# Performance work log

Hardware: AMD Instinct MI355X
Metric: run time of the kernel (lower is better)

The kernel has to match this reference:

```python
import jax, jax.numpy as jnp
import numpy as np

NUM_CLASSES = 101
BATCH = 262144
LAMBDA = 1000.0


def setup_inputs() -> dict:
    key = jax.random.key(0)
    k1, k2 = jax.random.split(key)
    outputs = jax.random.normal(k1, (BATCH, NUM_CLASSES), dtype=jnp.float32)
    targets = jax.random.randint(k2, (BATCH,), 0, NUM_CLASSES, dtype=jnp.int64)
    return {"outputs": outputs, "targets": targets}


def reference(outputs, targets):
    B, C = outputs.shape
    targets = targets.reshape(-1)
    tf = targets.astype(outputs.dtype)

    probs = jax.nn.softmax(outputs, axis=1)                      # [B, C]
    labels = jnp.arange(C, dtype=outputs.dtype)                  # [C]
    pred_values = jnp.sum(probs * labels[None, :], axis=1)       # [B]
    centered = labels[None, :] - pred_values[:, None]            # [B, C]
    variance = jnp.sum(probs * centered * centered, axis=1)      # [B]
    variance = jnp.clip(variance, 1e-6, None)
    est_err = (pred_values - tf) ** 2
    concentrated_loss = jnp.mean(0.5 * jnp.log(variance) + est_err / (2.0 * variance))

    # Unimodal ordinal penalty, vectorized over the original double loop:
    # sign_j = -1 if j < target else +1; penalty = relu(-(p_j - p_{j+1}) * sign_j)
    j = jnp.arange(C - 1)                                        # [C-1]
    sign = jnp.where(j[None, :] < targets[:, None], -1.0, 1.0).astype(outputs.dtype)
    prob_diff = probs[:, :-1] - probs[:, 1:]                     # [B, C-1]
    penalty = jax.nn.relu(-prob_diff * sign)
    unimodal_loss = jnp.sum(penalty) / B
    weighted_unimodal_loss = LAMBDA * unimodal_loss

    total_loss = concentrated_loss + weighted_unimodal_loss
    return (total_loss, concentrated_loss, weighted_unimodal_loss)
```

## Files before the change

### kernel.cpp

```cpp
#include <hip/hip_runtime.h>


#define NC 101
#define LAMBDA_W 1000.0

__global__ __launch_bounds__(256)
void ucl_stream_kernel(const float* __restrict__ x,
                       const int* __restrict__ tgt,
                       float2* __restrict__ partial,
                       int ngroups)
{
    const int tid  = threadIdx.x;
    const int lane = tid & 63;
    const int s    = lane & 15;
    const int gwave  = blockIdx.x * 4 + (tid >> 6);
    const int nwaves = gridDim.x * 4;

    float conc = 0.f, pens = 0.f;

    for (int g = gwave; g < ngroups; g += nwaves) {
        const int row = g * 4 + (lane >> 4);
        const float* __restrict__ xr = x + (size_t)row * NC;
        const int t = tgt[row];

        float e[7];
#pragma unroll
        for (int k = 0; k < 7; ++k) {
            const int j = s + 16 * k;
            e[k] = (j < NC) ? xr[j] : 0.f;
        }
#pragma unroll
        for (int k = 0; k < 7; ++k) {
            const int j = s + 16 * k;
            float ee = __expf(e[k]);
            e[k] = (j < NC) ? ee : 0.f;
        }

        float S = 0.f, W = 0.f, Q = 0.f;
#pragma unroll
        for (int k = 0; k < 7; ++k) {
            const float fj = (float)(s + 16 * k);
            S += e[k];
            W = fmaf(e[k], fj, W);
            Q = fmaf(e[k], fj * fj, Q);
        }

        float pen = 0.f;
#pragma unroll
        for (int k = 0; k < 7; ++k) {
            float n1 = __shfl_down(e[k], 1);
            float nx = (k < 6) ? __shfl(e[k + 1], lane & 48)
                               : 0.f;
            float en = (s == 15) ? nx : n1;
            float d  = e[k] - en;
            pen += fmaxf(d, 0.f);
            const int j = s + 16 * k;
            pen -= (j == t) ? e[k] : 0.f;
        }

#pragma unroll
        for (int off = 1; off < 16; off <<= 1) {
            S   += __shfl_xor(S, off);
            W   += __shfl_xor(W, off);
            Q   += __shfl_xor(Q, off);
            pen += __shfl_xor(pen, off);
        }

        if (s == 0) {
            float pred = W / S;
            float var  = fmaxf(fmaf(-pred, pred, Q / S), 1e-6f);
            float err  = pred - (float)t;
            conc += 0.5f * __logf(var) + err * err / (2.0f * var);
            pens += pen / S;
        }
    }

    conc += __shfl_down(conc, 16);
    pens += __shfl_down(pens, 16);
    conc += __shfl_down(conc, 32);
    pens += __shfl_down(pens, 32);

    __shared__ float red[8];
    if (lane == 0) {
        red[(tid >> 6) * 2 + 0] = conc;
        red[(tid >> 6) * 2 + 1] = pens;
    }
    __syncthreads();
    if (tid == 0)
        partial[blockIdx.x] = make_float2(red[0] + red[2] + red[4] + red[6],
                                          red[1] + red[3] + red[5] + red[7]);
}

__global__ __launch_bounds__(256)
void ucl_finalize(const float2* __restrict__ partial,
                  float* __restrict__ out,
                  int nblocks, double invB)
{
    const int tid = threadIdx.x;
    double c = 0.0, p = 0.0;
    for (int i = tid; i < nblocks; i += 256) {
        float2 v = partial[i];
        c += (double)v.x;
        p += (double)v.y;
    }
#pragma unroll
    for (int off = 32; off > 0; off >>= 1) {
        c += __shfl_down(c, off);
        p += __shfl_down(p, off);
    }
    __shared__ double sm[8];
    if ((tid & 63) == 0) { sm[(tid >> 6) * 2] = c; sm[(tid >> 6) * 2 + 1] = p; }
    __syncthreads();
    if (tid == 0) {
        double C = (sm[0] + sm[2] + sm[4] + sm[6]) * invB;
        double P = (sm[1] + sm[3] + sm[5] + sm[7]) * invB * LAMBDA_W;
        out[0] = (float)(C + P);
        out[1] = (float)C;
        out[2] = (float)P;
    }
}

extern "C" void kernel_launch(void* const* d_in, const int* in_sizes, int n_in,
                              void* d_out, int out_size, void* d_ws, size_t ws_size,
                              hipStream_t stream)
{
    const float* x   = (const float*)d_in[0];
    const int*   tgt = (const int*)d_in[1];
    float* out = (float*)d_out;
    float2* partial = (float2*)d_ws;

    const int B = in_sizes[1];
    const int ngroups = B / 4;
    const int blocks = 1024;

    hipLaunchKernelGGL(ucl_stream_kernel, dim3(blocks), dim3(256), 0, stream,
                       x, tgt, partial, ngroups);
    hipLaunchKernelGGL(ucl_finalize, dim3(1), dim3(256), 0, stream,
                       partial, out, blocks, 1.0 / (double)B);
}
```

Before: 154.6 us.

## Double-buffer row-group loads in registers and double the grid size

Restructures the grid-stride loop into a two-stage software pipeline. The next group's row values and target are loaded into a second register buffer while the current group is exponentiated and reduced, so global-load latency overlaps with compute. It also doubles the block count from 1024 to 2048 to put more waves in flight. The cost is higher register pressure from the extra seven-float buffer, which could reduce occupancy, plus twice as many partials for the finalize kernel to sum.

```diff
diff --git a/kernel.cpp b/kernel.cpp
--- a/kernel.cpp
+++ b/kernel.cpp
@@ -3,6 +3,73 @@
 
 #define NC 101
 #define LAMBDA_W 1000.0
+#define NBLK 2048
+
+__device__ __forceinline__ void load_group(const float* __restrict__ x,
+                                           const int* __restrict__ tgt,
+                                           int g, int team, int s,
+                                           float e[7], int& t)
+{
+    const int row = g * 4 + team;
+    const float* __restrict__ xr = x + (size_t)row * NC;
+#pragma unroll
+    for (int k = 0; k < 7; ++k) {
+        const int j = s + 16 * k;
+        e[k] = (j < NC) ? xr[j] : 0.f;
+    }
+    t = tgt[row];
+}
+
+__device__ __forceinline__ void compute_group(const float ein[7], int t,
+                                              int lane, int s,
+                                              float& conc, float& pens)
+{
+    float e[7];
+#pragma unroll
+    for (int k = 0; k < 7; ++k) {
+        const int j = s + 16 * k;
+        float ee = __expf(ein[k]);
+        e[k] = (j < NC) ? ee : 0.f;
+    }
+
+    float S = 0.f, W = 0.f, Q = 0.f;
+#pragma unroll
+    for (int k = 0; k < 7; ++k) {
+        const float fj = (float)(s + 16 * k);
+        S += e[k];
+        W = fmaf(e[k], fj, W);
+        Q = fmaf(e[k], fj * fj, Q);
+    }
+
+    float pen = 0.f;
+#pragma unroll
+    for (int k = 0; k < 7; ++k) {
+        float n1 = __shfl_down(e[k], 1);
+        float nx = (k < 6) ? __shfl(e[k + 1], lane & 48)
+                           : 0.f;
+        float en = (s == 15) ? nx : n1;
+        float d  = e[k] - en;
+        pen += fmaxf(d, 0.f);
+        const int j = s + 16 * k;
+        pen -= (j == t) ? e[k] : 0.f;
+    }
+
+#pragma unroll
+    for (int off = 1; off < 16; off <<= 1) {
+        S   += __shfl_xor(S, off);
+        W   += __shfl_xor(W, off);
+        Q   += __shfl_xor(Q, off);
+        pen += __shfl_xor(pen, off);
+    }
+
+    if (s == 0) {
+        float pred = W / S;
+        float var  = fmaxf(fmaf(-pred, pred, Q / S), 1e-6f);
+        float err  = pred - (float)t;
+        conc += 0.5f * __logf(var) + err * err / (2.0f * var);
+        pens += pen / S;
+    }
+}
 
 __global__ __launch_bounds__(256)
 void ucl_stream_kernel(const float* __restrict__ x,
@@ -13,66 +80,34 @@
     const int tid  = threadIdx.x;
     const int lane = tid & 63;
     const int s    = lane & 15;
+    const int team = lane >> 4;
     const int gwave  = blockIdx.x * 4 + (tid >> 6);
     const int nwaves = gridDim.x * 4;
 
     float conc = 0.f, pens = 0.f;
 
-    for (int g = gwave; g < ngroups; g += nwaves) {
-        const int row = g * 4 + (lane >> 4);
-        const float* __restrict__ xr = x + (size_t)row * NC;
-        const int t = tgt[row];
+    float eA[7], eB[7];
+    int tA = 0, tB = 0;
 
-        float e[7];
-#pragma unroll
-        for (int k = 0; k < 7; ++k) {
-            const int j = s + 16 * k;
-            e[k] = (j < NC) ? xr[j] : 0.f;
-        }
-#pragma unroll
-        for (int k = 0; k < 7; ++k) {
-            const int j = s + 16 * k;
-            float ee = __expf(e[k]);
-            e[k] = (j < NC) ? ee : 0.f;
-        }
+    int g = gwave;
+    bool haveA = (g < ngroups);
+    if (haveA)
+        load_group(x, tgt, g, team, s, eA, tA);
 
-        float S = 0.f, W = 0.f, Q = 0.f;
-#pragma unroll
-        for (int k = 0; k < 7; ++k) {
-            const float fj = (float)(s + 16 * k);
-            S += e[k];
-            W = fmaf(e[k], fj, W);
-            Q = fmaf(e[k], fj * fj, Q);
-        }
+    while (haveA) {
+        const int gB = g + nwaves;
+        const bool haveB = (gB < ngroups);
+        if (haveB)
+            load_group(x, tgt, gB, team, s, eB, tB);
+        compute_group(eA, tA, lane, s, conc, pens);
+        if (!haveB) break;
 
-        float pen = 0.f;
-#pragma unroll
-        for (int k = 0; k < 7; ++k) {
-            float n1 = __shfl_down(e[k], 1);
-            float nx = (k < 6) ? __shfl(e[k + 1], lane & 48)
-                               : 0.f;
-            float en = (s == 15) ? nx : n1;
-            float d  = e[k] - en;
-            pen += fmaxf(d, 0.f);
-            const int j = s + 16 * k;
-            pen -= (j == t) ? e[k] : 0.f;
-        }
-
-#pragma unroll
-        for (int off = 1; off < 16; off <<= 1) {
-            S   += __shfl_xor(S, off);
-            W   += __shfl_xor(W, off);
-            Q   += __shfl_xor(Q, off);
-            pen += __shfl_xor(pen, off);
-        }
-
-        if (s == 0) {
-            float pred = W / S;
-            float var  = fmaxf(fmaf(-pred, pred, Q / S), 1e-6f);
-            float err  = pred - (float)t;
-            conc += 0.5f * __logf(var) + err * err / (2.0f * var);
-            pens += pen / S;
-        }
+        const int gA2 = gB + nwaves;
+        haveA = (gA2 < ngroups);
+        if (haveA)
+            load_group(x, tgt, gA2, team, s, eA, tA);
+        compute_group(eB, tB, lane, s, conc, pens);
+        g = gA2;
     }
 
     conc += __shfl_down(conc, 16);
@@ -131,7 +166,7 @@
 
     const int B = in_sizes[1];
     const int ngroups = B / 4;
-    const int blocks = 1024;
+    const int blocks = NBLK;
 
     hipLaunchKernelGGL(ucl_stream_kernel, dim3(blocks), dim3(256), 0, stream,
                        x, tgt, partial, ngroups);
```

After: 161.4 us. +4.4%, slower.
